# Kernel tuning notes

Measured on AMD Instinct MI355X. Metric: run time of the kernel, lower is better.

Reference implementation:

```python
import jax, jax.numpy as jnp
import numpy as np
from jax import lax

WINDOW = 40          # plan.window_size
E = 8                # len(plan.expand_feature)
F = 64               # len(plan.feature)
OUT_CH = 128
KERNEL = 5
ALPHA = 0.01         # leaky_relu_alpha
N_LABEL = 1


def time_conv(x, conv_size):
    """x: [N, T, F] -> [N, WINDOW, 5*E] sliding-window stats over first E features."""
    N, T, _ = x.shape
    begin = T - (conv_size + WINDOW - 1)
    xe = x[:, :, :E]                                             # [N, T, E]
    idx = begin + jnp.arange(WINDOW)[:, None] + jnp.arange(conv_size)[None, :]  # [W, C]
    win = xe[:, idx, :]                                          # [N, W, C, E]
    _mean = win.mean(axis=2)                                     # [N, W, E]
    _std = jnp.std(win, axis=2, ddof=1)                          # torch.std is unbiased
    _max = win.max(axis=2)
    _min = win.min(axis=2)
    # rank of last timestep of each window, cross-sectionally over stocks (dim 0)
    last = xe[:, begin + conv_size - 1: begin + conv_size - 1 + WINDOW, :]  # [N, W, E]
    order = jnp.argsort(-last, axis=0)
    rank = jnp.argsort(order, axis=0).astype(x.dtype) / N        # [N, W, E]
    return jnp.concatenate([_mean, _std, rank, _max, _min], axis=2)  # [N, W, 5E]


def setup_inputs() -> dict:
    key = jax.random.key(0)
    k1, k2, k3, k4, k5 = jax.random.split(key, 5)
    N, T = 8000, 64
    in_ch = F + 10 * E  # 144
    x = jax.random.normal(k1, (N, T, F), dtype=jnp.float32)
    conv_w = jax.random.normal(k2, (OUT_CH, in_ch, KERNEL), dtype=jnp.float32) * 0.05
    conv_b = jax.random.normal(k3, (OUT_CH,), dtype=jnp.float32) * 0.05
    lin_in = WINDOW + 1 - KERNEL  # 36
    lin_w = jax.random.normal(k4, (N_LABEL, lin_in), dtype=jnp.float32) * 0.1
    lin_b = jax.random.normal(k5, (N_LABEL,), dtype=jnp.float32) * 0.1
    return {"x": x, "conv_w": conv_w, "conv_b": conv_b, "lin_w": lin_w, "lin_b": lin_b}


def reference(x, conv_w, conv_b, lin_w, lin_b):
    week_x = time_conv(x, conv_size=5)     # [N, W, 5E]
    month_x = time_conv(x, conv_size=20)   # [N, W, 5E]
    xc = jnp.concatenate([x[:, -WINDOW:, :], week_x, month_x], axis=2)  # [N, W, F+10E]
    cnn_x = jnp.transpose(xc, (0, 2, 1))   # [N, C, W]
    part = lax.conv_general_dilated(cnn_x, conv_w, window_strides=(1,),
                                    padding='VALID',
                                    dimension_numbers=('NCH', 'OIH', 'NCH'))
    part = part + conv_b[None, :, None]    # [N, OUT_CH, W+1-K]
    h = part[:, -1, :]                     # last output channel, [N, W+1-K]
    h = jnp.where(h >= 0, h, ALPHA * h)    # leaky relu
    return h @ lin_w.T + lin_b             # [N, N_LABEL]
```

## Files before the change

kernel.cpp:

```cpp
#include <hip/hip_runtime.h>
#include <math.h>

#define NS    8000
#define TT    64
#define FF    64
#define EE    8
#define WIN   40
#define TR    59
#define NBINS 8192

#define XET_SZ  (8*59*8000)
#define RNK_SZ  (8*40*8000)

__global__ __launch_bounds__(256) void k0(const float* __restrict__ x,
                                          const float* __restrict__ cw,
                                          float* __restrict__ xeT,
                                          float* __restrict__ uraw) {
    int n = blockIdx.x * 256 + threadIdx.x;
    int r = blockIdx.y;
    if (n >= NS) return;
    const float* row = x + (size_t)n * (TT * FF) + (5 + r) * FF;
    float4 a = *(const float4*)(row);
    float4 b = *(const float4*)(row + 4);
    xeT[(0 * TR + r) * NS + n] = a.x;
    xeT[(1 * TR + r) * NS + n] = a.y;
    xeT[(2 * TR + r) * NS + n] = a.z;
    xeT[(3 * TR + r) * NS + n] = a.w;
    xeT[(4 * TR + r) * NS + n] = b.x;
    xeT[(5 * TR + r) * NS + n] = b.y;
    xeT[(6 * TR + r) * NS + n] = b.z;
    xeT[(7 * TR + r) * NS + n] = b.w;

    if (r >= 19) {
        const int w = r - 19;
        const float* W = cw + 127 * 144 * 5;
        float4 v[16];
        v[0] = a; v[1] = b;
#pragma unroll
        for (int q = 2; q < 16; q++) v[q] = *(const float4*)(row + 4 * q);
        float acc0 = 0.f, acc1 = 0.f, acc2 = 0.f, acc3 = 0.f, acc4 = 0.f;
#pragma unroll
        for (int q = 0; q < 16; q++) {
            const float* Wq = W + (4 * q) * 5;
            acc0 += v[q].x * Wq[0]  + v[q].y * Wq[5]  + v[q].z * Wq[10] + v[q].w * Wq[15];
            acc1 += v[q].x * Wq[1]  + v[q].y * Wq[6]  + v[q].z * Wq[11] + v[q].w * Wq[16];
            acc2 += v[q].x * Wq[2]  + v[q].y * Wq[7]  + v[q].z * Wq[12] + v[q].w * Wq[17];
            acc3 += v[q].x * Wq[3]  + v[q].y * Wq[8]  + v[q].z * Wq[13] + v[q].w * Wq[18];
            acc4 += v[q].x * Wq[4]  + v[q].y * Wq[9]  + v[q].z * Wq[14] + v[q].w * Wq[19];
        }
        float* o = uraw + ((size_t)n * WIN + w) * 5;
        o[0] = acc0; o[1] = acc1; o[2] = acc2; o[3] = acc3; o[4] = acc4;
    }
}

__device__ __forceinline__ int binOf(float v) {
    int b = (int)((v + 4.0f) * 1024.0f);
    b = b < 0 ? 0 : b;
    return b > (NBINS - 1) ? (NBINS - 1) : b;
}

__device__ __forceinline__ unsigned long long keyOf(float v, unsigned idx) {
    unsigned s = __float_as_uint(v);
    unsigned m = (s & 0x80000000u) ? (~s) : (s | 0x80000000u);
    unsigned md = ~m;
    return ((unsigned long long)md << 13) | idx;
}

__global__ __launch_bounds__(1024) void k_rank(const float* __restrict__ xeT,
                                               float* __restrict__ rankT) {
    const int w = blockIdx.x;
    const int e = blockIdx.y;
    __shared__ unsigned hist[NBINS];
    __shared__ unsigned basev[NBINS];
    __shared__ unsigned long long sk[NS];
    __shared__ unsigned wsum[16];

    const int tid  = threadIdx.x;
    const int lane = tid & 63;
    const int wid  = tid >> 6;
    const float* col = xeT + ((size_t)e * TR + (19 + w)) * NS;

    float val[8];
#pragma unroll
    for (int i = 0; i < 8; i++) {
        int idx = tid + i * 1024;
        val[i] = (idx < NS) ? col[idx] : 0.0f;
    }
#pragma unroll
    for (int j = 0; j < 8; j++) hist[tid + j * 1024] = 0;
    __syncthreads();

#pragma unroll
    for (int i = 0; i < 8; i++) {
        int idx = tid + i * 1024;
        if (idx < NS) atomicAdd(&hist[binOf(val[i])], 1u);
    }
    __syncthreads();

    unsigned h[8];
#pragma unroll
    for (int j = 0; j < 8; j++) h[j] = hist[8 * tid + j];
    unsigned cs = 0;
#pragma unroll
    for (int j = 0; j < 8; j++) cs += h[j];
    unsigned sc = cs;
#pragma unroll
    for (int d = 1; d < 64; d <<= 1) {
        unsigned t2 = __shfl_up(sc, d);
        if (lane >= d) sc += t2;
    }
    if (lane == 63) wsum[wid] = sc;
    __syncthreads();
    unsigned woff = 0;
    for (int i = 0; i < wid; i++) woff += wsum[i];
    unsigned bsum = woff + (sc - cs);
#pragma unroll
    for (int j = 0; j < 8; j++) {
        int b = 8 * tid + j;
        unsigned bv = NS - bsum - h[j];
        basev[b] = bv;
        hist[b]  = bv;
        bsum += h[j];
    }
    __syncthreads();

#pragma unroll
    for (int i = 0; i < 8; i++) {
        int idx = tid + i * 1024;
        if (idx < NS) {
            int b = binOf(val[i]);
            unsigned p = atomicAdd(&hist[b], 1u);
            sk[p] = keyOf(val[i], (unsigned)idx);
        }
    }
    __syncthreads();

    float* outp = rankT + ((size_t)e * WIN + w) * NS;
#pragma unroll 1
    for (int i = 0; i < 8; i++) {
        int p = tid + i * 1024;
        if (p < NS) {
            unsigned long long k64 = sk[p];
            unsigned md = (unsigned)(k64 >> 13);
            unsigned m  = ~md;
            unsigned s  = (m & 0x80000000u) ? (m ^ 0x80000000u) : (~m);
            float v = __uint_as_float(s);
            int b = binOf(v);
            unsigned lo = basev[b];
            unsigned hi = (b == 0) ? NS : basev[b - 1];
            unsigned c = 0;
            for (unsigned q = lo; q < hi; q++) c += (sk[q] < k64);
            outp[k64 & 8191u] = (float)(basev[b] + c) * (1.0f / 8000.0f);
        }
    }
}

__global__ __launch_bounds__(256) void k_der_final(const float* __restrict__ cw,
                                                   const float* __restrict__ xeT,
                                                   const float* __restrict__ rankT,
                                                   const float* __restrict__ uraw,
                                                   const float* __restrict__ cb,
                                                   const float* __restrict__ lw,
                                                   const float* __restrict__ lb,
                                                   float* __restrict__ outp) {
    __shared__ float red[8][32][37];
    const int tid = threadIdx.x;
    const int e   = tid >> 5;
    const int nl  = tid & 31;
    const int n0  = blockIdx.x * 32;
    const int n   = n0 + nl;
    const float* W = cw + 127 * 144 * 5;

    float wm5[5], wsd5[5], wrk[5], wmx5[5], wmn5[5], wm20[5], wsd20[5], wmx20[5], wmn20[5];
#pragma unroll
    for (int k = 0; k < 5; k++) {
        wm5[k]   = W[(64  + e) * 5 + k];
        wsd5[k]  = W[(72  + e) * 5 + k];
        wrk[k]   = W[(80  + e) * 5 + k] + W[(120 + e) * 5 + k];
        wmx5[k]  = W[(88  + e) * 5 + k];
        wmn5[k]  = W[(96  + e) * 5 + k];
        wm20[k]  = W[(104 + e) * 5 + k];
        wsd20[k] = W[(112 + e) * 5 + k];
        wmx20[k] = W[(128 + e) * 5 + k];
        wmn20[k] = W[(136 + e) * 5 + k];
    }

    float gder[36];
#pragma unroll
    for (int j = 0; j < 36; j++) gder[j] = 0.0f;

    const float* col = xeT + (size_t)e * TR * NS + n;
    const float* rkp = rankT + (size_t)e * WIN * NS + n;

    float ring[20];
#pragma unroll
    for (int r = 0; r < 19; r++) ring[r] = col[(size_t)r * NS];

#pragma unroll
    for (int w = 0; w < WIN; w++) {
        ring[(w + 19) % 20] = col[(size_t)(w + 19) * NS];
        float s20 = 0.f, mn20 = ring[0], mx20 = ring[0];
#pragma unroll
        for (int i = 0; i < 20; i++) {
            float v = ring[i];
            s20 += v; mn20 = fminf(mn20, v); mx20 = fmaxf(mx20, v);
        }
        float m20 = s20 * (1.0f / 20.0f);
        float d20 = 0.f;
#pragma unroll
        for (int i = 0; i < 20; i++) { float t = ring[i] - m20; d20 += t * t; }
        float sd20 = sqrtf(d20 * (1.0f / 19.0f));

        float s5 = 0.f, mn5 = ring[(w + 15) % 20], mx5 = mn5;
#pragma unroll
        for (int i = 15; i < 20; i++) {
            float v = ring[(w + i) % 20];
            s5 += v; mn5 = fminf(mn5, v); mx5 = fmaxf(mx5, v);
        }
        float m5 = s5 * 0.2f;
        float d5 = 0.f;
#pragma unroll
        for (int i = 15; i < 20; i++) {
            float t = ring[(w + i) % 20] - m5; d5 += t * t;
        }
        float sd5 = sqrtf(d5 * 0.25f);

        float rk = rkp[(size_t)w * NS];

#pragma unroll
        for (int k = 0; k < 5; k++) {
            int j = w - k;
            if (j >= 0 && j < 36) {
                float uk;
                uk  = m5   * wm5[k];
                uk += sd5  * wsd5[k];
                uk += rk   * wrk[k];
                uk += mx5  * wmx5[k];
                uk += mn5  * wmn5[k];
                uk += m20  * wm20[k];
                uk += sd20 * wsd20[k];
                uk += mx20 * wmx20[k];
                uk += mn20 * wmn20[k];
                gder[j] += uk;
            }
        }
    }

#pragma unroll
    for (int j = 0; j < 36; j++) red[e][nl][j] = gder[j];
    __syncthreads();

    for (int p = tid; p < 32 * 36; p += 256) {
        int nl2 = p / 36, j = p - nl2 * 36;
        float sum = 0.f;
#pragma unroll
        for (int e2 = 0; e2 < 8; e2++) sum += red[e2][nl2][j];
        red[0][nl2][j] = sum;
    }
    __syncthreads();

    if (tid < 32) {
        const float* ur = uraw + (size_t)n * (WIN * 5);
        float b127 = cb[127];
        float acc = lb[0];
#pragma unroll
        for (int j = 0; j < 36; j++) {
            float g = b127 + red[0][tid][j];
#pragma unroll
            for (int k = 0; k < 5; k++) g += ur[(j + k) * 5 + k];
            g = (g >= 0.0f) ? g : 0.01f * g;
            acc += g * lw[j];
        }
        outp[n] = acc;
    }
}

extern "C" void kernel_launch(void* const* d_in, const int* in_sizes, int n_in,
                              void* d_out, int out_size, void* d_ws, size_t ws_size,
                              hipStream_t stream) {
    const float* x  = (const float*)d_in[0];
    const float* cw = (const float*)d_in[1];
    const float* cb = (const float*)d_in[2];
    const float* lw = (const float*)d_in[3];
    const float* lb = (const float*)d_in[4];
    float* outp = (float*)d_out;

    float* ws    = (float*)d_ws;
    float* xeT   = ws;
    float* rankT = ws + XET_SZ;
    float* uraw  = ws + XET_SZ + RNK_SZ;

    k0<<<dim3(32, 59), 256, 0, stream>>>(x, cw, xeT, uraw);
    k_rank<<<dim3(WIN, EE), 1024, 0, stream>>>(xeT, rankT);
    k_der_final<<<250, 256, 0, stream>>>(cw, xeT, rankT, uraw, cb, lw, lb, outp);
}
```

Measured before the change: 244.7 us.

## Compact rank-kernel shared memory and write ranks coalesced via shared scatter

The cross-sectional rank kernel now keeps sorted keys as separate float values and 16-bit indices instead of 64-bit packed keys, and stores bin bases as shorts. It halves the histogram bins and runs 512 threads per block. The total shared-memory footprint falls enough to fit more blocks per CU. Computed ranks are first scattered into shared memory by original index, so the global store becomes a contiguous coalesced write instead of a random scatter. In exchange, the coarser bins roughly double the within-bin comparison loop, and each thread handles twice as many elements.

```diff
diff --git a/kernel.cpp b/kernel.cpp
--- a/kernel.cpp
+++ b/kernel.cpp
@@ -7,7 +7,7 @@
 #define EE    8
 #define WIN   40
 #define TR    59
-#define NBINS 8192
+#define NBINS 4096
 
 #define XET_SZ  (8*59*8000)
 #define RNK_SZ  (8*40*8000)
@@ -54,45 +54,39 @@
 }
 
 __device__ __forceinline__ int binOf(float v) {
-    int b = (int)((v + 4.0f) * 1024.0f);
+    int b = (int)((v + 4.0f) * 512.0f);
     b = b < 0 ? 0 : b;
     return b > (NBINS - 1) ? (NBINS - 1) : b;
 }
 
-__device__ __forceinline__ unsigned long long keyOf(float v, unsigned idx) {
-    unsigned s = __float_as_uint(v);
-    unsigned m = (s & 0x80000000u) ? (~s) : (s | 0x80000000u);
-    unsigned md = ~m;
-    return ((unsigned long long)md << 13) | idx;
-}
-
-__global__ __launch_bounds__(1024) void k_rank(const float* __restrict__ xeT,
-                                               float* __restrict__ rankT) {
+__global__ __launch_bounds__(512, 4) void k_rank(const float* __restrict__ xeT,
+                                                 float* __restrict__ rankT) {
     const int w = blockIdx.x;
     const int e = blockIdx.y;
     __shared__ unsigned hist[NBINS];
-    __shared__ unsigned basev[NBINS];
-    __shared__ unsigned long long sk[NS];
-    __shared__ unsigned wsum[16];
+    __shared__ unsigned short basev[NBINS];
+    __shared__ float          sk[NS];
+    __shared__ unsigned short si[NS];
+    __shared__ unsigned wsum[8];
 
     const int tid  = threadIdx.x;
     const int lane = tid & 63;
     const int wid  = tid >> 6;
     const float* col = xeT + ((size_t)e * TR + (19 + w)) * NS;
 
-    float val[8];
-#pragma unroll
-    for (int i = 0; i < 8; i++) {
-        int idx = tid + i * 1024;
+    float val[16];
+#pragma unroll
+    for (int i = 0; i < 16; i++) {
+        int idx = tid + i * 512;
         val[i] = (idx < NS) ? col[idx] : 0.0f;
     }
 #pragma unroll
-    for (int j = 0; j < 8; j++) hist[tid + j * 1024] = 0;
-    __syncthreads();
-
-#pragma unroll
-    for (int i = 0; i < 8; i++) {
-        int idx = tid + i * 1024;
+    for (int j = 0; j < 8; j++) hist[tid + j * 512] = 0;
+    __syncthreads();
+
+#pragma unroll
+    for (int i = 0; i < 16; i++) {
+        int idx = tid + i * 512;
         if (idx < NS) atomicAdd(&hist[binOf(val[i])], 1u);
     }
     __syncthreads();
@@ -118,40 +112,60 @@
     for (int j = 0; j < 8; j++) {
         int b = 8 * tid + j;
         unsigned bv = NS - bsum - h[j];
-        basev[b] = bv;
+        basev[b] = (unsigned short)bv;
         hist[b]  = bv;
         bsum += h[j];
     }
     __syncthreads();
 
 #pragma unroll
-    for (int i = 0; i < 8; i++) {
-        int idx = tid + i * 1024;
+    for (int i = 0; i < 16; i++) {
+        int idx = tid + i * 512;
         if (idx < NS) {
             int b = binOf(val[i]);
             unsigned p = atomicAdd(&hist[b], 1u);
-            sk[p] = keyOf(val[i], (unsigned)idx);
-        }
-    }
-    __syncthreads();
-
-    float* outp = rankT + ((size_t)e * WIN + w) * NS;
+            sk[p] = val[i];
+            si[p] = (unsigned short)idx;
+        }
+    }
+    __syncthreads();
+
+    unsigned packed[16];
 #pragma unroll 1
-    for (int i = 0; i < 8; i++) {
-        int p = tid + i * 1024;
+    for (int i = 0; i < 16; i++) {
+        int p = tid + i * 512;
+        packed[i] = 0xFFFFFFFFu;
         if (p < NS) {
-            unsigned long long k64 = sk[p];
-            unsigned md = (unsigned)(k64 >> 13);
-            unsigned m  = ~md;
-            unsigned s  = (m & 0x80000000u) ? (m ^ 0x80000000u) : (~m);
-            float v = __uint_as_float(s);
+            float v = sk[p];
+            unsigned idm = si[p];
             int b = binOf(v);
             unsigned lo = basev[b];
-            unsigned hi = (b == 0) ? NS : basev[b - 1];
+            unsigned hi = (b == 0) ? NS : (unsigned)basev[b - 1];
             unsigned c = 0;
-            for (unsigned q = lo; q < hi; q++) c += (sk[q] < k64);
-            outp[k64 & 8191u] = (float)(basev[b] + c) * (1.0f / 8000.0f);
-        }
+            for (unsigned q = lo; q < hi; q++) {
+                float u2 = sk[q];
+                if (u2 > v) c++;
+                else if (u2 == v) {
+                    if (si[q] < idm) c++;
+                }
+            }
+            packed[i] = (idm << 16) | ((unsigned)basev[b] + c);
+        }
+    }
+    __syncthreads();
+
+#pragma unroll
+    for (int i = 0; i < 16; i++) {
+        if (packed[i] != 0xFFFFFFFFu)
+            si[packed[i] >> 16] = (unsigned short)(packed[i] & 0xFFFFu);
+    }
+    __syncthreads();
+
+    float* outp = rankT + ((size_t)e * WIN + w) * NS;
+#pragma unroll
+    for (int i = 0; i < 16; i++) {
+        int t = tid + i * 512;
+        if (t < NS) outp[t] = (float)si[t] * (1.0f / 8000.0f);
     }
 }
 
@@ -291,6 +305,6 @@
     float* uraw  = ws + XET_SZ + RNK_SZ;
 
     k0<<<dim3(32, 59), 256, 0, stream>>>(x, cw, xeT, uraw);
-    k_rank<<<dim3(WIN, EE), 1024, 0, stream>>>(xeT, rankT);
+    k_rank<<<dim3(WIN, EE), 512, 0, stream>>>(xeT, rankT);
     k_der_final<<<250, 256, 0, stream>>>(cw, xeT, rankT, uraw, cb, lw, lb, outp);
 }
```

Result: slower. 254.2 us (+3.9%).
